# Optimization experiments

Hardware: AMD Instinct MI355X
Metric: run time of the kernel (lower is better)

## Reference

```python
import jax, jax.numpy as jnp
import numpy as np

B, F, D = 16384, 64, 32
H = 256            # deep_intermediate_size
HO = 128           # higher_order_features_size
NPAIR = F * (F - 1) // 2
CIN = HO + NPAIR + D
OUT = 1


def setup_inputs() -> dict:
    key = jax.random.key(0)
    ks = jax.random.split(key, 12)
    s = 0.02
    return {
        'x':   jax.random.normal(ks[0], (B, F, D), jnp.float32),
        'W1':  jax.random.normal(ks[1], (F * D, H), jnp.float32) * s,
        'b1':  jnp.zeros((H,), jnp.float32),
        'W2':  jax.random.normal(ks[2], (H, H), jnp.float32) * s,
        'b2':  jnp.zeros((H,), jnp.float32),
        'W3':  jax.random.normal(ks[3], (H, HO), jnp.float32) * s,
        'b3':  jnp.zeros((HO,), jnp.float32),
        'Wc1': jax.random.normal(ks[4], (CIN, 256), jnp.float32) * s,
        'bc1': jnp.zeros((256,), jnp.float32),
        'Wc2': jax.random.normal(ks[5], (256, OUT), jnp.float32) * s,
        'bc2': jnp.zeros((OUT,), jnp.float32),
    }


def reference(x, W1, b1, W2, b2, W3, b3, Wc1, bc1, Wc2, bc2):
    b, f, d = x.shape
    # second-order interactions: Gram matrix + upper-triangular extraction
    # (replaces the O(F^2) python loop of bmm's in the original)
    gram = jnp.einsum('bid,bjd->bij', x, x)          # (B, F, F)
    iu, ju = jnp.triu_indices(f, k=1)                # row-major i<j order, matches the loop
    soi = gram[:, iu, ju]                            # (B, F*(F-1)/2)
    # original writes so_int into a fresh non-grad tensor -> detached
    soi = jax.lax.stop_gradient(soi)

    # deep processor (3-layer MLP with SELU; dropout inactive at eval)
    h = jax.nn.selu(x.reshape(b, f * d) @ W1 + b1)
    h = jax.nn.selu(h @ W2 + b2)
    hoi = h @ W3 + b3                                # (B, HO)

    first_order = x.sum(axis=1)                      # (B, D)

    cin = jnp.concatenate([hoi, soi, first_order], axis=1)  # (B, CIN)
    c = jax.nn.relu(cin @ Wc1 + bc1)
    return c @ Wc2 + bc2                             # (B, OUT)
```

## Files before the change

### kernel.cpp

```cpp
#include <hip/hip_runtime.h>
#include <hip/hip_bf16.h>

#define BATCH 16384
#define F_DIM 64
#define D_DIM 32
#define H_DIM 256
#define HO_DIM 128
#define NPAIR 2016
#define CIN_DIM 2176

typedef __hip_bfloat16 bf16;
using bf16x8 = __attribute__((ext_vector_type(8))) __bf16;
using f32x4  = __attribute__((ext_vector_type(4))) float;

__device__ inline float selu_f(float v) {
    const float scale = 1.0507009873554805f;
    const float alpha = 1.6732632423543772f;
    return v > 0.f ? scale * v : scale * alpha * (__expf(v) - 1.f);
}

__device__ inline void gload16(const void* g, void* l) {
    __builtin_amdgcn_global_load_lds(
        (const __attribute__((address_space(1))) void*)g,
        (__attribute__((address_space(3))) void*)l,
        16, 0, 0);
}

__global__ void transpose_cvt(const float* __restrict__ in, bf16* __restrict__ out,
                              int K, int N, int logN) {
    int i = blockIdx.x * 256 + threadIdx.x;
    if (i >= K * N) return;
    int n = i & (N - 1), k = i >> logN;
    out[(size_t)n * K + k] = __float2bfloat16(in[i]);
}

__global__ __launch_bounds__(256) void gram_first(const float* __restrict__ x,
                                                  bf16* __restrict__ cin) {
    __shared__ __align__(16) bf16 stage[4][NPAIR];
    int w = threadIdx.x >> 6, l = threadIdx.x & 63;
    int b = blockIdx.x * 4 + w;
    const float* X = x + (size_t)b * (F_DIM * D_DIM);
    int lr = l & 15, lk = l >> 4;

    bf16x8 xa[4];
    float fsum[8];
#pragma unroll
    for (int j = 0; j < 8; ++j) fsum[j] = 0.f;

#pragma unroll
    for (int ti = 0; ti < 4; ++ti) {
        const float* p = X + (ti * 16 + lr) * D_DIM + lk * 8;
        float4 f0 = *(const float4*)p;
        float4 f1 = *(const float4*)(p + 4);
        bf16x8 t;
        t[0] = (__bf16)f0.x; t[1] = (__bf16)f0.y; t[2] = (__bf16)f0.z; t[3] = (__bf16)f0.w;
        t[4] = (__bf16)f1.x; t[5] = (__bf16)f1.y; t[6] = (__bf16)f1.z; t[7] = (__bf16)f1.w;
        xa[ti] = t;
        fsum[0] += f0.x; fsum[1] += f0.y; fsum[2] += f0.z; fsum[3] += f0.w;
        fsum[4] += f1.x; fsum[5] += f1.y; fsum[6] += f1.z; fsum[7] += f1.w;
    }

    const int pi[10] = {0,0,0,0,1,1,1,2,2,3};
    const int pj[10] = {0,1,2,3,1,2,3,2,3,3};
    f32x4 zero = {0.f, 0.f, 0.f, 0.f};
#pragma unroll
    for (int p = 0; p < 10; ++p) {
        f32x4 g = __builtin_amdgcn_mfma_f32_16x16x32_bf16(xa[pi[p]], xa[pj[p]], zero, 0, 0, 0);
        int ib = pi[p] * 16 + lk * 4;
        int j  = pj[p] * 16 + lr;
#pragma unroll
        for (int r = 0; r < 4; ++r) {
            int i = ib + r;
            if (j > i) {
                int idx = (i * (127 - i)) / 2 + (j - i - 1);
                stage[w][idx] = __float2bfloat16(g[r]);
            }
        }
    }

#pragma unroll
    for (int m = 1; m < 16; m <<= 1)
#pragma unroll
        for (int j = 0; j < 8; ++j)
            fsum[j] += __shfl_xor(fsum[j], m, 64);
    if (lr == 0) {
        bf16* dst = cin + (size_t)b * CIN_DIM + (HO_DIM + NPAIR) + lk * 8;
#pragma unroll
        for (int j = 0; j < 8; ++j) dst[j] = __float2bfloat16(fsum[j]);
    }

    __syncthreads();
    const uint4* s4 = (const uint4*)&stage[0][0];
    int base_b = blockIdx.x * 4;
    for (int c = threadIdx.x; c < 4 * 252; c += 256) {
        int bb = c / 252, off = c - bb * 252;
        uint4 v = s4[c];
        *(uint4*)(cin + (size_t)(base_b + bb) * CIN_DIM + HO_DIM + off * 8) = v;
    }
}

template<int K, int N, int ACT, bool AFP32>
__global__ __launch_bounds__(512) void gemm_lds(
    const void* __restrict__ Av,
    const bf16* __restrict__ BT,
    const float* __restrict__ bias,
    bf16* __restrict__ C, int ldc, int ccol,
    const float* __restrict__ Wc2, const float* __restrict__ bc2,
    float* __restrict__ Out)
{
    constexpr int BK = 64;
    constexpr int NT = K / BK;
    constexpr int FN = N / 64;
    constexpr int BST = (N * 8) / 512;

    __shared__ __align__(16) bf16 Abuf[2][64 * BK];
    __shared__ __align__(16) bf16 Bbuf[2][N * BK];
    __shared__ float red[4][64];

    const int tid = threadIdx.x;
    const int w = tid >> 6, l = tid & 63;
    const int wm = w >> 2, wn = w & 3;
    const int lr = l & 15, lk = l >> 4;
    const int rowblk = blockIdx.x * 64;

    const int srow = tid >> 3, sks = tid & 7;

    const bf16*  gAb = (const bf16*)Av  + (size_t)(rowblk + srow) * K + ((sks ^ (srow & 7)) * 8);
    const float* gAf = (const float*)Av + (size_t)(rowblk + srow) * K + ((sks ^ (srow & 7)) * 8);

    const bf16* gBs[BST];
#pragma unroll
    for (int s = 0; s < BST; ++s) {
        int col = s * 64 + srow;
        gBs[s] = BT + (size_t)col * K + ((sks ^ (col & 7)) * 8);
    }

    int aoff[2][2], boff[FN][2];
#pragma unroll
    for (int fm = 0; fm < 2; ++fm) {
        int arow = wm * 32 + fm * 16 + lr;
#pragma unroll
        for (int kk = 0; kk < 2; ++kk)
            aoff[fm][kk] = arow * BK + (((kk * 4 + lk) ^ (arow & 7)) * 8);
    }
#pragma unroll
    for (int fn = 0; fn < FN; ++fn) {
        int bcol = wn * (FN * 16) + fn * 16 + lr;
#pragma unroll
        for (int kk = 0; kk < 2; ++kk)
            boff[fn][kk] = bcol * BK + (((kk * 4 + lk) ^ (bcol & 7)) * 8);
    }

    f32x4 acc[2][FN];
#pragma unroll
    for (int fm = 0; fm < 2; ++fm)
#pragma unroll
        for (int fn = 0; fn < FN; ++fn)
            acc[fm][fn] = (f32x4){0.f, 0.f, 0.f, 0.f};

    float4 pA0, pA1;
    auto stage = [&](int buf, int t) {
        if constexpr (AFP32) {
            const float* p = gAf + (size_t)t * BK;
            pA0 = *(const float4*)p;
            pA1 = *(const float4*)(p + 4);
        } else {
            gload16(gAb + (size_t)t * BK, &Abuf[buf][tid * 8]);
        }
#pragma unroll
        for (int s = 0; s < BST; ++s)
            gload16(gBs[s] + (size_t)t * BK, &Bbuf[buf][(s * 512 + tid) * 8]);
    };
    auto commitA = [&](int buf) {
        if constexpr (AFP32) {
            bf16x8 v;
            v[0] = (__bf16)pA0.x; v[1] = (__bf16)pA0.y; v[2] = (__bf16)pA0.z; v[3] = (__bf16)pA0.w;
            v[4] = (__bf16)pA1.x; v[5] = (__bf16)pA1.y; v[6] = (__bf16)pA1.z; v[7] = (__bf16)pA1.w;
            *(bf16x8*)&Abuf[buf][tid * 8] = v;
        }
    };

    stage(0, 0);
    commitA(0);
    __syncthreads();

    int cur = 0;
    for (int t = 0; t < NT; ++t) {
        if (t + 1 < NT) stage(cur ^ 1, t + 1);

        bf16x8 a[2][2], bfr[FN][2];
#pragma unroll
        for (int fm = 0; fm < 2; ++fm)
#pragma unroll
            for (int kk = 0; kk < 2; ++kk)
                a[fm][kk] = *(const bf16x8*)&Abuf[cur][aoff[fm][kk]];
#pragma unroll
        for (int fn = 0; fn < FN; ++fn)
#pragma unroll
            for (int kk = 0; kk < 2; ++kk)
                bfr[fn][kk] = *(const bf16x8*)&Bbuf[cur][boff[fn][kk]];

#pragma unroll
        for (int kk = 0; kk < 2; ++kk)
#pragma unroll
            for (int fm = 0; fm < 2; ++fm)
#pragma unroll
                for (int fn = 0; fn < FN; ++fn)
                    acc[fm][fn] = __builtin_amdgcn_mfma_f32_16x16x32_bf16(
                        a[fm][kk], bfr[fn][kk], acc[fm][fn], 0, 0, 0);

        if (t + 1 < NT) commitA(cur ^ 1);
        __syncthreads();
        cur ^= 1;
    }

    if constexpr (ACT == 2) {
        float part[2][4];
#pragma unroll
        for (int fm = 0; fm < 2; ++fm)
#pragma unroll
            for (int r = 0; r < 4; ++r) part[fm][r] = 0.f;
#pragma unroll
        for (int fm = 0; fm < 2; ++fm) {
#pragma unroll
            for (int fn = 0; fn < FN; ++fn) {
                int col = wn * (FN * 16) + fn * 16 + lr;
                float bv = bias[col];
                float wv = Wc2[col];
#pragma unroll
                for (int r = 0; r < 4; ++r) {
                    float v = acc[fm][fn][r] + bv;
                    v = fmaxf(v, 0.f);
                    part[fm][r] += v * wv;
                }
            }
        }
#pragma unroll
        for (int fm = 0; fm < 2; ++fm)
#pragma unroll
            for (int r = 0; r < 4; ++r)
#pragma unroll
                for (int m = 1; m < 16; m <<= 1)
                    part[fm][r] += __shfl_xor(part[fm][r], m, 64);
        if (lr == 0) {
#pragma unroll
            for (int fm = 0; fm < 2; ++fm)
#pragma unroll
                for (int r = 0; r < 4; ++r)
                    red[wn][wm * 32 + fm * 16 + lk * 4 + r] = part[fm][r];
        }
        __syncthreads();
        if (tid < 64)
            Out[rowblk + tid] = red[0][tid] + red[1][tid] + red[2][tid] + red[3][tid] + bc2[0];
    } else {
#pragma unroll
        for (int fm = 0; fm < 2; ++fm) {
#pragma unroll
            for (int fn = 0; fn < FN; ++fn) {
                int col = wn * (FN * 16) + fn * 16 + lr;
                float bv = bias[col];
#pragma unroll
                for (int r = 0; r < 4; ++r) {
                    float v = acc[fm][fn][r] + bv;
                    if constexpr (ACT == 1) v = selu_f(v);
                    int row = rowblk + wm * 32 + fm * 16 + lk * 4 + r;
                    C[(size_t)row * ldc + ccol + col] = __float2bfloat16(v);
                }
            }
        }
    }
}

extern "C" void kernel_launch(void* const* d_in, const int* in_sizes, int n_in,
                              void* d_out, int out_size, void* d_ws, size_t ws_size,
                              hipStream_t stream) {
    const float* x   = (const float*)d_in[0];
    const float* W1  = (const float*)d_in[1];
    const float* b1  = (const float*)d_in[2];
    const float* W2  = (const float*)d_in[3];
    const float* b2  = (const float*)d_in[4];
    const float* W3  = (const float*)d_in[5];
    const float* b3  = (const float*)d_in[6];
    const float* Wc1 = (const float*)d_in[7];
    const float* bc1 = (const float*)d_in[8];
    const float* Wc2 = (const float*)d_in[9];
    const float* bc2 = (const float*)d_in[10];
    float* out = (float*)d_out;

    char* ws = (char*)d_ws;
    bf16* W1T  = (bf16*)ws; ws += (size_t)2048 * 256 * 2;
    bf16* W2T  = (bf16*)ws; ws += (size_t)256 * 256 * 2;
    bf16* W3T  = (bf16*)ws; ws += (size_t)128 * 256 * 2;
    bf16* Wc1T = (bf16*)ws; ws += (size_t)256 * 2176 * 2;
    bf16* h1   = (bf16*)ws; ws += (size_t)BATCH * H_DIM * 2;
    bf16* h2   = (bf16*)ws; ws += (size_t)BATCH * H_DIM * 2;
    bf16* cin  = (bf16*)ws; ws += (size_t)BATCH * CIN_DIM * 2;

    transpose_cvt<<<2048, 256, 0, stream>>>(W1, W1T, 2048, 256, 8);
    transpose_cvt<<<256,  256, 0, stream>>>(W2, W2T, 256, 256, 8);
    transpose_cvt<<<128,  256, 0, stream>>>(W3, W3T, 256, 128, 7);
    transpose_cvt<<<2176, 256, 0, stream>>>(Wc1, Wc1T, 2176, 256, 8);

    gram_first<<<4096, 256, 0, stream>>>(x, cin);

    gemm_lds<2048, 256, 1, true><<<256, 512, 0, stream>>>(x, W1T, b1, h1, 256, 0,
                                                          nullptr, nullptr, nullptr);
    gemm_lds<256, 256, 1, false><<<256, 512, 0, stream>>>(h1, W2T, b2, h2, 256, 0,
                                                          nullptr, nullptr, nullptr);
    gemm_lds<256, 128, 0, false><<<256, 512, 0, stream>>>(h2, W3T, b3, cin, CIN_DIM, 0,
                                                          nullptr, nullptr, nullptr);
    gemm_lds<2176, 256, 2, false><<<256, 512, 0, stream>>>(cin, Wc1T, bc1, nullptr, 0, 0,
                                                           Wc2, bc2, out);
}
```

Before: 152.9 us.

## Fuse gram with first MLP layer, fuse layers two and three, merge weight prep

```diff
diff --git a/kernel.cpp b/kernel.cpp
--- a/kernel.cpp
+++ b/kernel.cpp
@@ -26,85 +26,370 @@
         16, 0, 0);
 }
 
-__global__ void transpose_cvt(const float* __restrict__ in, bf16* __restrict__ out,
-                              int K, int N, int logN) {
-    int i = blockIdx.x * 256 + threadIdx.x;
-    if (i >= K * N) return;
-    int n = i & (N - 1), k = i >> logN;
-    out[(size_t)n * K + k] = __float2bfloat16(in[i]);
-}
-
-__global__ __launch_bounds__(256) void gram_first(const float* __restrict__ x,
-                                                  bf16* __restrict__ cin) {
-    __shared__ __align__(16) bf16 stage[4][NPAIR];
-    int w = threadIdx.x >> 6, l = threadIdx.x & 63;
-    int b = blockIdx.x * 4 + w;
-    const float* X = x + (size_t)b * (F_DIM * D_DIM);
-    int lr = l & 15, lk = l >> 4;
-
-    bf16x8 xa[4];
-    float fsum[8];
-#pragma unroll
-    for (int j = 0; j < 8; ++j) fsum[j] = 0.f;
-
-#pragma unroll
-    for (int ti = 0; ti < 4; ++ti) {
-        const float* p = X + (ti * 16 + lr) * D_DIM + lk * 8;
-        float4 f0 = *(const float4*)p;
-        float4 f1 = *(const float4*)(p + 4);
-        bf16x8 t;
-        t[0] = (__bf16)f0.x; t[1] = (__bf16)f0.y; t[2] = (__bf16)f0.z; t[3] = (__bf16)f0.w;
-        t[4] = (__bf16)f1.x; t[5] = (__bf16)f1.y; t[6] = (__bf16)f1.z; t[7] = (__bf16)f1.w;
-        xa[ti] = t;
-        fsum[0] += f0.x; fsum[1] += f0.y; fsum[2] += f0.z; fsum[3] += f0.w;
-        fsum[4] += f1.x; fsum[5] += f1.y; fsum[6] += f1.z; fsum[7] += f1.w;
-    }
-
+__global__ void prep(const float* __restrict__ W1, const float* __restrict__ W2,
+                     const float* __restrict__ W3, const float* __restrict__ Wc1,
+                     bf16* __restrict__ W1T, bf16* __restrict__ W2T,
+                     bf16* __restrict__ W3Tsw, bf16* __restrict__ Wc1T) {
+    int bid = blockIdx.x, tid = threadIdx.x;
+    if (bid < 2048) {
+        int i = bid * 256 + tid;
+        int n = i & 255, k = i >> 8;
+        W1T[(size_t)n * 2048 + k] = __float2bfloat16(W1[i]);
+    } else if (bid < 2304) {
+        int i = (bid - 2048) * 256 + tid;
+        int n = i & 255, k = i >> 8;
+        W2T[n * 256 + k] = __float2bfloat16(W2[i]);
+    } else if (bid < 2432) {
+        int i = (bid - 2304) * 256 + tid;
+        int k = i >> 7, n = i & 127;
+        W3Tsw[n * 256 + (((k >> 3) ^ (n & 7)) * 8) + (k & 7)] = __float2bfloat16(W3[i]);
+    } else {
+        int i = (bid - 2432) * 256 + tid;
+        int n = i & 255, k = i >> 8;
+        Wc1T[(size_t)n * 2176 + k] = __float2bfloat16(Wc1[i]);
+    }
+}
+
+__global__ __launch_bounds__(512, 2) void gram_mlp1(
+    const float* __restrict__ x, const bf16* __restrict__ W1T,
+    const float* __restrict__ b1, bf16* __restrict__ cin, bf16* __restrict__ h1) {
+    constexpr int K = 2048;
+    __shared__ __align__(16) char smraw[81920];
+    bf16* Abuf0 = (bf16*)smraw;
+    bf16* Abuf1 = (bf16*)(smraw + 8192);
+    bf16* Bbuf0 = (bf16*)(smraw + 16384);
+    bf16* Bbuf1 = (bf16*)(smraw + 49152);
+
+    const int tid = threadIdx.x;
+    const int w = tid >> 6, l = tid & 63;
+    const int lr = l & 15, lk = l >> 4;
+    const int wm = w >> 2, wn = w & 3;
+    const int blk = blockIdx.x;
+    const int batch0 = blk * 64 + w * 8;
+
+    bf16x8 xa[8][4];
+    bf16* mysoi = (bf16*)(smraw + w * 4096);
     const int pi[10] = {0,0,0,0,1,1,1,2,2,3};
     const int pj[10] = {0,1,2,3,1,2,3,2,3,3};
-    f32x4 zero = {0.f, 0.f, 0.f, 0.f};
-#pragma unroll
-    for (int p = 0; p < 10; ++p) {
-        f32x4 g = __builtin_amdgcn_mfma_f32_16x16x32_bf16(xa[pi[p]], xa[pj[p]], zero, 0, 0, 0);
-        int ib = pi[p] * 16 + lk * 4;
-        int j  = pj[p] * 16 + lr;
-#pragma unroll
-        for (int r = 0; r < 4; ++r) {
-            int i = ib + r;
-            if (j > i) {
-                int idx = (i * (127 - i)) / 2 + (j - i - 1);
-                stage[w][idx] = __float2bfloat16(g[r]);
+
+    float4 pf[2][8];
+#pragma unroll
+    for (int ti = 0; ti < 4; ++ti) {
+        const float* p = x + (size_t)batch0 * 2048 + (ti * 16 + lr) * 32 + lk * 8;
+        pf[0][ti * 2]     = *(const float4*)p;
+        pf[0][ti * 2 + 1] = *(const float4*)(p + 4);
+    }
+
+#pragma unroll
+    for (int bb = 0; bb < 8; ++bb) {
+        if (bb < 7) {
+#pragma unroll
+            for (int ti = 0; ti < 4; ++ti) {
+                const float* p = x + (size_t)(batch0 + bb + 1) * 2048 + (ti * 16 + lr) * 32 + lk * 8;
+                pf[(bb + 1) & 1][ti * 2]     = *(const float4*)p;
+                pf[(bb + 1) & 1][ti * 2 + 1] = *(const float4*)(p + 4);
             }
         }
-    }
-
-#pragma unroll
-    for (int m = 1; m < 16; m <<= 1)
-#pragma unroll
-        for (int j = 0; j < 8; ++j)
-            fsum[j] += __shfl_xor(fsum[j], m, 64);
-    if (lr == 0) {
-        bf16* dst = cin + (size_t)b * CIN_DIM + (HO_DIM + NPAIR) + lk * 8;
-#pragma unroll
-        for (int j = 0; j < 8; ++j) dst[j] = __float2bfloat16(fsum[j]);
+        float fsum[8];
+#pragma unroll
+        for (int j = 0; j < 8; ++j) fsum[j] = 0.f;
+#pragma unroll
+        for (int ti = 0; ti < 4; ++ti) {
+            float4 f0 = pf[bb & 1][ti * 2];
+            float4 f1 = pf[bb & 1][ti * 2 + 1];
+            bf16x8 t;
+            t[0] = (__bf16)f0.x; t[1] = (__bf16)f0.y; t[2] = (__bf16)f0.z; t[3] = (__bf16)f0.w;
+            t[4] = (__bf16)f1.x; t[5] = (__bf16)f1.y; t[6] = (__bf16)f1.z; t[7] = (__bf16)f1.w;
+            xa[bb][ti] = t;
+            fsum[0] += f0.x; fsum[1] += f0.y; fsum[2] += f0.z; fsum[3] += f0.w;
+            fsum[4] += f1.x; fsum[5] += f1.y; fsum[6] += f1.z; fsum[7] += f1.w;
+        }
+#pragma unroll
+        for (int m = 1; m < 16; m <<= 1)
+#pragma unroll
+            for (int j = 0; j < 8; ++j)
+                fsum[j] += __shfl_xor(fsum[j], m, 64);
+        if (lr == 0) {
+            bf16x8 fv;
+#pragma unroll
+            for (int j = 0; j < 8; ++j) fv[j] = (__bf16)fsum[j];
+            *(bf16x8*)(cin + (size_t)(batch0 + bb) * CIN_DIM + (HO_DIM + NPAIR) + lk * 8) = fv;
+        }
+        f32x4 zero = {0.f, 0.f, 0.f, 0.f};
+#pragma unroll
+        for (int p = 0; p < 10; ++p) {
+            f32x4 g = __builtin_amdgcn_mfma_f32_16x16x32_bf16(xa[bb][pi[p]], xa[bb][pj[p]], zero, 0, 0, 0);
+            int ib = pi[p] * 16 + lk * 4;
+            int j  = pj[p] * 16 + lr;
+#pragma unroll
+            for (int r = 0; r < 4; ++r) {
+                int i = ib + r;
+                if (j > i) {
+                    int idx = (i * (127 - i)) / 2 + (j - i - 1);
+                    mysoi[idx] = __float2bfloat16(g[r]);
+                }
+            }
+        }
+        const uint4* s4 = (const uint4*)mysoi;
+        uint4* dst = (uint4*)(cin + (size_t)(batch0 + bb) * CIN_DIM + HO_DIM);
+        for (int c = l; c < 252; c += 64) dst[c] = s4[c];
     }
 
     __syncthreads();
-    const uint4* s4 = (const uint4*)&stage[0][0];
-    int base_b = blockIdx.x * 4;
-    for (int c = threadIdx.x; c < 4 * 252; c += 256) {
-        int bb = c / 252, off = c - bb * 252;
-        uint4 v = s4[c];
-        *(uint4*)(cin + (size_t)(base_b + bb) * CIN_DIM + HO_DIM + off * 8) = v;
-    }
-}
-
-template<int K, int N, int ACT, bool AFP32>
-__global__ __launch_bounds__(512) void gemm_lds(
-    const void* __restrict__ Av,
+
+    const bf16* gBs[4];
+#pragma unroll
+    for (int s = 0; s < 4; ++s) {
+        int col = s * 64 + (tid >> 3);
+        gBs[s] = W1T + (size_t)col * K + (((tid & 7) ^ (col & 7)) * 8);
+    }
+    int aoff[2][2], boff[4][2];
+#pragma unroll
+    for (int fm = 0; fm < 2; ++fm) {
+        int arow = wm * 32 + fm * 16 + lr;
+#pragma unroll
+        for (int kk = 0; kk < 2; ++kk)
+            aoff[fm][kk] = arow * 64 + (((kk * 4 + lk) ^ (arow & 7)) * 8);
+    }
+#pragma unroll
+    for (int fn = 0; fn < 4; ++fn) {
+        int bcol = wn * 64 + fn * 16 + lr;
+#pragma unroll
+        for (int kk = 0; kk < 2; ++kk)
+            boff[fn][kk] = bcol * 64 + (((kk * 4 + lk) ^ (bcol & 7)) * 8);
+    }
+
+    f32x4 acc[2][4];
+#pragma unroll
+    for (int fm = 0; fm < 2; ++fm)
+#pragma unroll
+        for (int fn = 0; fn < 4; ++fn)
+            acc[fm][fn] = (f32x4){0.f, 0.f, 0.f, 0.f};
+
+#define WRITEA(tt, DST) { \
+    const int f0_ = 2 * (tt); \
+    const int lrA_ = f0_ & 15, lrB_ = (f0_ + 1) & 15; \
+    int delta_ = (lr == lrA_) ? 0 : ((lr == lrB_) ? 1 : -1); \
+    if (delta_ >= 0) { \
+        int cs_ = delta_ * 4 + lk; \
+        _Pragma("unroll") \
+        for (int bb_ = 0; bb_ < 8; ++bb_) { \
+            int row_ = w * 8 + bb_; \
+            *(bf16x8*)((DST) + row_ * 64 + ((cs_ ^ (row_ & 7)) * 8)) = xa[bb_][(tt) >> 3]; \
+        } } }
+
+    WRITEA(0, Abuf0);
+#pragma unroll
+    for (int s = 0; s < 4; ++s)
+        gload16(gBs[s], Bbuf0 + (s * 512 + tid) * 8);
+    __syncthreads();
+
+#pragma unroll
+    for (int t = 0; t < 32; ++t) {
+        bf16* Ac = (t & 1) ? Abuf1 : Abuf0;
+        bf16* Bc = (t & 1) ? Bbuf1 : Bbuf0;
+        bf16* An = (t & 1) ? Abuf0 : Abuf1;
+        bf16* Bn = (t & 1) ? Bbuf0 : Bbuf1;
+        if (t < 31) {
+#pragma unroll
+            for (int s = 0; s < 4; ++s)
+                gload16(gBs[s] + (size_t)(t + 1) * 64, Bn + (s * 512 + tid) * 8);
+        }
+        bf16x8 a[2][2], bfr[4][2];
+#pragma unroll
+        for (int fm = 0; fm < 2; ++fm)
+#pragma unroll
+            for (int kk = 0; kk < 2; ++kk)
+                a[fm][kk] = *(const bf16x8*)(Ac + aoff[fm][kk]);
+#pragma unroll
+        for (int fn = 0; fn < 4; ++fn)
+#pragma unroll
+            for (int kk = 0; kk < 2; ++kk)
+                bfr[fn][kk] = *(const bf16x8*)(Bc + boff[fn][kk]);
+#pragma unroll
+        for (int kk = 0; kk < 2; ++kk)
+#pragma unroll
+            for (int fm = 0; fm < 2; ++fm)
+#pragma unroll
+                for (int fn = 0; fn < 4; ++fn)
+                    acc[fm][fn] = __builtin_amdgcn_mfma_f32_16x16x32_bf16(
+                        a[fm][kk], bfr[fn][kk], acc[fm][fn], 0, 0, 0);
+        if (t < 31) WRITEA(t + 1, An);
+        __syncthreads();
+    }
+#undef WRITEA
+
+#pragma unroll
+    for (int fm = 0; fm < 2; ++fm) {
+#pragma unroll
+        for (int fn = 0; fn < 4; ++fn) {
+            int col = wn * 64 + fn * 16 + lr;
+            float bv = b1[col];
+#pragma unroll
+            for (int r = 0; r < 4; ++r) {
+                float v = selu_f(acc[fm][fn][r] + bv);
+                int row = blk * 64 + wm * 32 + fm * 16 + lk * 4 + r;
+                h1[(size_t)row * 256 + col] = __float2bfloat16(v);
+            }
+        }
+    }
+}
+
+__global__ __launch_bounds__(512, 2) void mlp23(
+    const bf16* __restrict__ h1, const bf16* __restrict__ W2T, const float* __restrict__ b2,
+    const bf16* __restrict__ W3Tsw, const float* __restrict__ b3, bf16* __restrict__ cin) {
+    __shared__ __align__(16) char smraw[147456];
+    bf16* Abuf0 = (bf16*)smraw;
+    bf16* Abuf1 = (bf16*)(smraw + 8192);
+    bf16* Bbuf0 = (bf16*)(smraw + 16384);
+    bf16* Bbuf1 = (bf16*)(smraw + 49152);
+    bf16* w3l   = (bf16*)(smraw + 81920);
+    bf16* h2sw  = (bf16*)smraw;
+
+    const int tid = threadIdx.x;
+    const int w = tid >> 6, l = tid & 63;
+    const int lr = l & 15, lk = l >> 4;
+    const int wm = w >> 2, wn = w & 3;
+    const int rowblk = blockIdx.x * 64;
+    const int srow = tid >> 3, sks = tid & 7;
+
+#pragma unroll
+    for (int s = 0; s < 8; ++s)
+        gload16(W3Tsw + (size_t)(s * 512 + tid) * 8, w3l + (s * 512 + tid) * 8);
+
+    const bf16* gA = h1 + (size_t)(rowblk + srow) * 256 + ((sks ^ (srow & 7)) * 8);
+    const bf16* gBs[4];
+#pragma unroll
+    for (int s = 0; s < 4; ++s) {
+        int col = s * 64 + srow;
+        gBs[s] = W2T + (size_t)col * 256 + ((sks ^ (col & 7)) * 8);
+    }
+    int aoff[2][2], boff[4][2];
+#pragma unroll
+    for (int fm = 0; fm < 2; ++fm) {
+        int arow = wm * 32 + fm * 16 + lr;
+#pragma unroll
+        for (int kk = 0; kk < 2; ++kk)
+            aoff[fm][kk] = arow * 64 + (((kk * 4 + lk) ^ (arow & 7)) * 8);
+    }
+#pragma unroll
+    for (int fn = 0; fn < 4; ++fn) {
+        int bcol = wn * 64 + fn * 16 + lr;
+#pragma unroll
+        for (int kk = 0; kk < 2; ++kk)
+            boff[fn][kk] = bcol * 64 + (((kk * 4 + lk) ^ (bcol & 7)) * 8);
+    }
+
+    f32x4 acc[2][4];
+#pragma unroll
+    for (int fm = 0; fm < 2; ++fm)
+#pragma unroll
+        for (int fn = 0; fn < 4; ++fn)
+            acc[fm][fn] = (f32x4){0.f, 0.f, 0.f, 0.f};
+
+    gload16(gA, Abuf0 + tid * 8);
+#pragma unroll
+    for (int s = 0; s < 4; ++s)
+        gload16(gBs[s], Bbuf0 + (s * 512 + tid) * 8);
+    __syncthreads();
+
+#pragma unroll
+    for (int t = 0; t < 4; ++t) {
+        bf16* Ac = (t & 1) ? Abuf1 : Abuf0;
+        bf16* Bc = (t & 1) ? Bbuf1 : Bbuf0;
+        bf16* An = (t & 1) ? Abuf0 : Abuf1;
+        bf16* Bn = (t & 1) ? Bbuf0 : Bbuf1;
+        if (t < 3) {
+            gload16(gA + (size_t)(t + 1) * 64, An + tid * 8);
+#pragma unroll
+            for (int s = 0; s < 4; ++s)
+                gload16(gBs[s] + (size_t)(t + 1) * 64, Bn + (s * 512 + tid) * 8);
+        }
+        bf16x8 a[2][2], bfr[4][2];
+#pragma unroll
+        for (int fm = 0; fm < 2; ++fm)
+#pragma unroll
+            for (int kk = 0; kk < 2; ++kk)
+                a[fm][kk] = *(const bf16x8*)(Ac + aoff[fm][kk]);
+#pragma unroll
+        for (int fn = 0; fn < 4; ++fn)
+#pragma unroll
+            for (int kk = 0; kk < 2; ++kk)
+                bfr[fn][kk] = *(const bf16x8*)(Bc + boff[fn][kk]);
+#pragma unroll
+        for (int kk = 0; kk < 2; ++kk)
+#pragma unroll
+            for (int fm = 0; fm < 2; ++fm)
+#pragma unroll
+                for (int fn = 0; fn < 4; ++fn)
+                    acc[fm][fn] = __builtin_amdgcn_mfma_f32_16x16x32_bf16(
+                        a[fm][kk], bfr[fn][kk], acc[fm][fn], 0, 0, 0);
+        __syncthreads();
+    }
+
+#pragma unroll
+    for (int fm = 0; fm < 2; ++fm) {
+#pragma unroll
+        for (int fn = 0; fn < 4; ++fn) {
+            int col = wn * 64 + fn * 16 + lr;
+            float bv = b2[col];
+#pragma unroll
+            for (int r = 0; r < 4; ++r) {
+                float v = selu_f(acc[fm][fn][r] + bv);
+                int row = wm * 32 + fm * 16 + lk * 4 + r;
+                h2sw[row * 256 + (((col >> 3) ^ (row & 7)) * 8) + (col & 7)] = __float2bfloat16(v);
+            }
+        }
+    }
+    __syncthreads();
+
+    f32x4 acc2[2][2];
+#pragma unroll
+    for (int fm = 0; fm < 2; ++fm)
+#pragma unroll
+        for (int fn = 0; fn < 2; ++fn)
+            acc2[fm][fn] = (f32x4){0.f, 0.f, 0.f, 0.f};
+#pragma unroll
+    for (int ks = 0; ks < 8; ++ks) {
+        bf16x8 a2[2], b2f[2];
+#pragma unroll
+        for (int fm = 0; fm < 2; ++fm) {
+            int arow = wm * 32 + fm * 16 + lr;
+            a2[fm] = *(const bf16x8*)(h2sw + arow * 256 + (((ks * 4 + lk) ^ (arow & 7)) * 8));
+        }
+#pragma unroll
+        for (int fn = 0; fn < 2; ++fn) {
+            int ncol = wn * 32 + fn * 16 + lr;
+            b2f[fn] = *(const bf16x8*)(w3l + ncol * 256 + (((ks * 4 + lk) ^ (ncol & 7)) * 8));
+        }
+#pragma unroll
+        for (int fm = 0; fm < 2; ++fm)
+#pragma unroll
+            for (int fn = 0; fn < 2; ++fn)
+                acc2[fm][fn] = __builtin_amdgcn_mfma_f32_16x16x32_bf16(
+                    a2[fm], b2f[fn], acc2[fm][fn], 0, 0, 0);
+    }
+#pragma unroll
+    for (int fm = 0; fm < 2; ++fm) {
+#pragma unroll
+        for (int fn = 0; fn < 2; ++fn) {
+            int col = wn * 32 + fn * 16 + lr;
+            float bv = b3[col];
+#pragma unroll
+            for (int r = 0; r < 4; ++r) {
+                float v = acc2[fm][fn][r] + bv;
+                int row = rowblk + wm * 32 + fm * 16 + lk * 4 + r;
+                cin[(size_t)row * CIN_DIM + col] = __float2bfloat16(v);
+            }
+        }
+    }
+}
+
+template<int K, int N>
+__global__ __launch_bounds__(512) void gemm_head(
+    const bf16* __restrict__ A,
     const bf16* __restrict__ BT,
     const float* __restrict__ bias,
-    bf16* __restrict__ C, int ldc, int ccol,
     const float* __restrict__ Wc2, const float* __restrict__ bc2,
     float* __restrict__ Out)
 {
@@ -122,12 +407,9 @@
     const int wm = w >> 2, wn = w & 3;
     const int lr = l & 15, lk = l >> 4;
     const int rowblk = blockIdx.x * 64;
-
     const int srow = tid >> 3, sks = tid & 7;
 
-    const bf16*  gAb = (const bf16*)Av  + (size_t)(rowblk + srow) * K + ((sks ^ (srow & 7)) * 8);
-    const float* gAf = (const float*)Av + (size_t)(rowblk + srow) * K + ((sks ^ (srow & 7)) * 8);
-
+    const bf16* gAb = A + (size_t)(rowblk + srow) * K + ((sks ^ (srow & 7)) * 8);
     const bf16* gBs[BST];
 #pragma unroll
     for (int s = 0; s < BST; ++s) {
@@ -158,36 +440,19 @@
         for (int fn = 0; fn < FN; ++fn)
             acc[fm][fn] = (f32x4){0.f, 0.f, 0.f, 0.f};
 
-    float4 pA0, pA1;
     auto stage = [&](int buf, int t) {
-        if constexpr (AFP32) {
-            const float* p = gAf + (size_t)t * BK;
-            pA0 = *(const float4*)p;
-            pA1 = *(const float4*)(p + 4);
-        } else {
-            gload16(gAb + (size_t)t * BK, &Abuf[buf][tid * 8]);
-        }
+        gload16(gAb + (size_t)t * BK, &Abuf[buf][tid * 8]);
 #pragma unroll
         for (int s = 0; s < BST; ++s)
             gload16(gBs[s] + (size_t)t * BK, &Bbuf[buf][(s * 512 + tid) * 8]);
     };
-    auto commitA = [&](int buf) {
-        if constexpr (AFP32) {
-            bf16x8 v;
-            v[0] = (__bf16)pA0.x; v[1] = (__bf16)pA0.y; v[2] = (__bf16)pA0.z; v[3] = (__bf16)pA0.w;
-            v[4] = (__bf16)pA1.x; v[5] = (__bf16)pA1.y; v[6] = (__bf16)pA1.z; v[7] = (__bf16)pA1.w;
-            *(bf16x8*)&Abuf[buf][tid * 8] = v;
-        }
-    };
 
     stage(0, 0);
-    commitA(0);
     __syncthreads();
 
     int cur = 0;
     for (int t = 0; t < NT; ++t) {
         if (t + 1 < NT) stage(cur ^ 1, t + 1);
-
         bf16x8 a[2][2], bfr[FN][2];
 #pragma unroll
         for (int fm = 0; fm < 2; ++fm)
@@ -199,7 +464,6 @@
 #pragma unroll
             for (int kk = 0; kk < 2; ++kk)
                 bfr[fn][kk] = *(const bf16x8*)&Bbuf[cur][boff[fn][kk]];
-
 #pragma unroll
         for (int kk = 0; kk < 2; ++kk)
 #pragma unroll
@@ -208,67 +472,47 @@
                 for (int fn = 0; fn < FN; ++fn)
                     acc[fm][fn] = __builtin_amdgcn_mfma_f32_16x16x32_bf16(
                         a[fm][kk], bfr[fn][kk], acc[fm][fn], 0, 0, 0);
-
-        if (t + 1 < NT) commitA(cur ^ 1);
         __syncthreads();
         cur ^= 1;
     }
 
-    if constexpr (ACT == 2) {
-        float part[2][4];
+    float part[2][4];
+#pragma unroll
+    for (int fm = 0; fm < 2; ++fm)
+#pragma unroll
+        for (int r = 0; r < 4; ++r) part[fm][r] = 0.f;
+#pragma unroll
+    for (int fm = 0; fm < 2; ++fm) {
+#pragma unroll
+        for (int fn = 0; fn < FN; ++fn) {
+            int col = wn * (FN * 16) + fn * 16 + lr;
+            float bv = bias[col];
+            float wv = Wc2[col];
+#pragma unroll
+            for (int r = 0; r < 4; ++r) {
+                float v = acc[fm][fn][r] + bv;
+                v = fmaxf(v, 0.f);
+                part[fm][r] += v * wv;
+            }
+        }
+    }
+#pragma unroll
+    for (int fm = 0; fm < 2; ++fm)
+#pragma unroll
+        for (int r = 0; r < 4; ++r)
+#pragma unroll
+            for (int m = 1; m < 16; m <<= 1)
+                part[fm][r] += __shfl_xor(part[fm][r], m, 64);
+    if (lr == 0) {
 #pragma unroll
         for (int fm = 0; fm < 2; ++fm)
 #pragma unroll
-            for (int r = 0; r < 4; ++r) part[fm][r] = 0.f;
-#pragma unroll
-        for (int fm = 0; fm < 2; ++fm) {
-#pragma unroll
-            for (int fn = 0; fn < FN; ++fn) {
-                int col = wn * (FN * 16) + fn * 16 + lr;
-                float bv = bias[col];
-                float wv = Wc2[col];
-#pragma unroll
-                for (int r = 0; r < 4; ++r) {
-                    float v = acc[fm][fn][r] + bv;
-                    v = fmaxf(v, 0.f);
-                    part[fm][r] += v * wv;
-                }
-            }
-        }
-#pragma unroll
-        for (int fm = 0; fm < 2; ++fm)
-#pragma unroll
             for (int r = 0; r < 4; ++r)
-#pragma unroll
-                for (int m = 1; m < 16; m <<= 1)
-                    part[fm][r] += __shfl_xor(part[fm][r], m, 64);
-        if (lr == 0) {
-#pragma unroll
-            for (int fm = 0; fm < 2; ++fm)
-#pragma unroll
-                for (int r = 0; r < 4; ++r)
-                    red[wn][wm * 32 + fm * 16 + lk * 4 + r] = part[fm][r];
-        }
-        __syncthreads();
-        if (tid < 64)
-            Out[rowblk + tid] = red[0][tid] + red[1][tid] + red[2][tid] + red[3][tid] + bc2[0];
-    } else {
-#pragma unroll
-        for (int fm = 0; fm < 2; ++fm) {
-#pragma unroll
-            for (int fn = 0; fn < FN; ++fn) {
-                int col = wn * (FN * 16) + fn * 16 + lr;
-                float bv = bias[col];
-#pragma unroll
-                for (int r = 0; r < 4; ++r) {
-                    float v = acc[fm][fn][r] + bv;
-                    if constexpr (ACT == 1) v = selu_f(v);
-                    int row = rowblk + wm * 32 + fm * 16 + lk * 4 + r;
-                    C[(size_t)row * ldc + ccol + col] = __float2bfloat16(v);
-                }
-            }
-        }
-    }
+                red[wn][wm * 32 + fm * 16 + lk * 4 + r] = part[fm][r];
+    }
+    __syncthreads();
+    if (tid < 64)
+        Out[rowblk + tid] = red[0][tid] + red[1][tid] + red[2][tid] + red[3][tid] + bc2[0];
 }
 
 extern "C" void kernel_launch(void* const* d_in, const int* in_sizes, int n_in,
@@ -288,27 +532,15 @@
     float* out = (float*)d_out;
 
     char* ws = (char*)d_ws;
-    bf16* W1T  = (bf16*)ws; ws += (size_t)2048 * 256 * 2;
-    bf16* W2T  = (bf16*)ws; ws += (size_t)256 * 256 * 2;
-    bf16* W3T  = (bf16*)ws; ws += (size_t)128 * 256 * 2;
-    bf16* Wc1T = (bf16*)ws; ws += (size_t)256 * 2176 * 2;
-    bf16* h1   = (bf16*)ws; ws += (size_t)BATCH * H_DIM * 2;
-    bf16* h2   = (bf16*)ws; ws += (size_t)BATCH * H_DIM * 2;
-    bf16* cin  = (bf16*)ws; ws += (size_t)BATCH * CIN_DIM * 2;
-
-    transpose_cvt<<<2048, 256, 0, stream>>>(W1, W1T, 2048, 256, 8);
-    transpose_cvt<<<256,  256, 0, stream>>>(W2, W2T, 256, 256, 8);
-    transpose_cvt<<<128,  256, 0, stream>>>(W3, W3T, 256, 128, 7);
-    transpose_cvt<<<2176, 256, 0, stream>>>(Wc1, Wc1T, 2176, 256, 8);
-
-    gram_first<<<4096, 256, 0, stream>>>(x, cin);
-
-    gemm_lds<2048, 256, 1, true><<<256, 512, 0, stream>>>(x, W1T, b1, h1, 256, 0,
-                                                          nullptr, nullptr, nullptr);
-    gemm_lds<256, 256, 1, false><<<256, 512, 0, stream>>>(h1, W2T, b2, h2, 256, 0,
-                                                          nullptr, nullptr, nullptr);
-    gemm_lds<256, 128, 0, false><<<256, 512, 0, stream>>>(h2, W3T, b3, cin, CIN_DIM, 0,
-                                                          nullptr, nullptr, nullptr);
-    gemm_lds<2176, 256, 2, false><<<256, 512, 0, stream>>>(cin, Wc1T, bc1, nullptr, 0, 0,
-                                                           Wc2, bc2, out);
-}
+    bf16* W1T   = (bf16*)ws; ws += (size_t)256 * 2048 * 2;
+    bf16* W2T   = (bf16*)ws; ws += (size_t)256 * 256 * 2;
+    bf16* W3Tsw = (bf16*)ws; ws += (size_t)128 * 256 * 2;
+    bf16* Wc1T  = (bf16*)ws; ws += (size_t)256 * 2176 * 2;
+    bf16* h1    = (bf16*)ws; ws += (size_t)BATCH * H_DIM * 2;
+    bf16* cin   = (bf16*)ws; ws += (size_t)BATCH * CIN_DIM * 2;
+
+    prep<<<4608, 256, 0, stream>>>(W1, W2, W3, Wc1, W1T, W2T, W3Tsw, Wc1T);
+    gram_mlp1<<<256, 512, 0, stream>>>(x, W1T, b1, cin, h1);
+    mlp23<<<256, 512, 0, stream>>>(h1, W2T, b2, W3Tsw, b3, cin);
+    gemm_head<2176, 256><<<256, 512, 0, stream>>>(cin, Wc1T, bc1, Wc2, bc2, out);
+}
```

Measured after the change: 123.3 us. 1.24x faster.
